# Performance work log

Measured on AMD Instinct MI355X. Metric: run time of the kernel, lower is better.

The kernel has to match this reference:

```python
import jax, jax.numpy as jnp
import numpy as np

HEADS = 8

def _grid_edges(H, W):
    # 4-neighbor grid adjacency, built at trace time (static), faithful to the torch double loop
    N = H * W
    idx = np.arange(N).reshape(H, W)
    e = np.zeros((N, N), np.float32)
    a, b = idx[1:, :].ravel(), idx[:-1, :].ravel()
    e[a, b] = 1.0; e[b, a] = 1.0
    a, b = idx[:, 1:].ravel(), idx[:, :-1].ravel()
    e[a, b] = 1.0; e[b, a] = 1.0
    return jnp.asarray(e)

def _layernorm(x, g, b, eps=1e-5):
    m = x.mean(-1, keepdims=True)
    v = x.var(-1, keepdims=True)
    return (x - m) / jnp.sqrt(v + eps) * g + b

def _gat(nodes, edges, W, b, rel):
    # nodes: [N,B,E]; W: [4,E,E] (q,k,v,out); rel: [HEADS]
    N, B, E = nodes.shape
    hd = E // HEADS
    q = (nodes @ W[0].T + b[0]).reshape(N, B, HEADS, hd)
    k = (nodes @ W[1].T + b[1]).reshape(N, B, HEADS, hd)
    v = (nodes @ W[2].T + b[2]).reshape(N, B, HEADS, hd)
    s = jnp.einsum('ibhd,jbhd->hbij', q, k) / float(np.sqrt(hd))
    s = s + edges[None, None] * rel[:, None, None, None]  # per-head edge relation bias
    a = jax.nn.softmax(s, axis=1)  # faithful to source: softmax over dim=1 (batch axis)
    o = jnp.einsum('hbij,jbhd->ibhd', a, v).reshape(N, B, E)
    return o @ W[3].T + b[3]

def _mha(q_in, kv_in, W, b):
    # standard nn.MultiheadAttention (eval, no dropout); seq-first [L,B,E]
    L, B, E = q_in.shape
    S = kv_in.shape[0]
    hd = E // HEADS
    q = (q_in @ W[0].T + b[0]).reshape(L, B, HEADS, hd)
    k = (kv_in @ W[1].T + b[1]).reshape(S, B, HEADS, hd)
    v = (kv_in @ W[2].T + b[2]).reshape(S, B, HEADS, hd)
    s = jnp.einsum('ibhd,jbhd->hbij', q, k) / float(np.sqrt(hd))
    a = jax.nn.softmax(s, axis=-1)
    o = jnp.einsum('hbij,jbhd->ibhd', a, v).reshape(L, B, E)
    return o @ W[3].T + b[3]

def reference(x, gat_W, gat_b, gat_rel, cross_W, cross_b, ln_g, ln_b):
    B, C, H, W = x.shape
    P = H // 4
    # global nodes: avg_pool2d(kernel=4) then flatten to [P*P, B, C]
    g = x.reshape(B, C, P, 4, P, 4).mean(axis=(3, 5))
    global_nodes = g.reshape(B, C, P * P).transpose(2, 0, 1)
    global_edges = jnp.ones((P * P, P * P), x.dtype)
    local_nodes = x.reshape(B, C, H * W).transpose(2, 0, 1)  # [HW,B,C]
    local_edges = _grid_edges(H, W)
    g_out = _gat(global_nodes, global_edges, gat_W[0], gat_b[0], gat_rel[0])
    g_out = _layernorm(g_out + global_nodes, ln_g[0], ln_b[0])
    l_out = _gat(local_nodes, local_edges, gat_W[1], gat_b[1], gat_rel[1])
    l_out = _layernorm(l_out + local_nodes, ln_g[1], ln_b[1])
    # nearest upsample x4 of global output back to HxW
    g_map = g_out.transpose(1, 2, 0).reshape(B, C, P, P)
    g_up = jnp.repeat(jnp.repeat(g_map, 4, axis=2), 4, axis=3)
    g_up = g_up.reshape(B, C, H * W).transpose(2, 0, 1)
    c_out = _mha(l_out, g_up, cross_W, cross_b)
    c_out = _layernorm(c_out + l_out, ln_g[2], ln_b[2])
    return c_out.transpose(1, 2, 0).reshape(B, C, H, W)

def setup_inputs() -> dict:
    key = jax.random.key(0)
    ks = jax.random.split(key, 6)
    B, C, H, W = 2, 256, 40, 40
    E = C
    sc = 0.02
    return {
        "x": jax.random.normal(ks[0], (B, C, H, W), jnp.float32),
        "gat_W": jax.random.normal(ks[1], (2, 4, E, E), jnp.float32) * sc,
        "gat_b": jax.random.normal(ks[2], (2, 4, E), jnp.float32) * sc,
        "gat_rel": jax.random.normal(ks[3], (2, HEADS), jnp.float32),
        "cross_W": jax.random.normal(ks[4], (4, E, E), jnp.float32) * sc,
        "cross_b": jax.random.normal(ks[5], (4, E), jnp.float32) * sc,
        "ln_g": jnp.ones((3, E), jnp.float32),
        "ln_b": jnp.zeros((3, E), jnp.float32),
    }
```

## Files before the change

kernel.cpp:

```cpp
#include <hip/hip_runtime.h>
#include <math.h>

#define NLOC 1600
#define NGLO 100

typedef unsigned short u16;
typedef short s16x8 __attribute__((ext_vector_type(8)));
typedef float f32x4 __attribute__((ext_vector_type(4)));

__device__ __forceinline__ short f2bf(float f) {
    unsigned u = __float_as_uint(f);
    u += 0x7fffu + ((u >> 16) & 1u);
    return (short)(u >> 16);
}
__device__ __forceinline__ float bf2f(u16 h) {
    return __uint_as_float(((unsigned)h) << 16);
}


__device__ __forceinline__ void gemm_tile(int lane, const u16* __restrict__ A,
                                          const u16* __restrict__ W,
                                          const float* __restrict__ bias,
                                          u16* __restrict__ C, int M, int m0, int n0) {
    int c = lane & 15, qd = lane >> 4;
    f32x4 acc[2][4] = {};
#pragma unroll 2
    for (int kc = 0; kc < 8; ++kc) {
        int ko = kc * 32 + qd * 8;
        s16x8 af[2], bf[4];
#pragma unroll
        for (int mi = 0; mi < 2; ++mi) {
            int row = m0 + mi * 16 + c;
            s16x8 zz = {};
            af[mi] = (row < M) ? *(const s16x8*)(A + (size_t)row * 256 + ko) : zz;
        }
#pragma unroll
        for (int ni = 0; ni < 4; ++ni)
            bf[ni] = *(const s16x8*)(W + (size_t)(n0 + ni * 16 + c) * 256 + ko);
#pragma unroll
        for (int mi = 0; mi < 2; ++mi)
#pragma unroll
            for (int ni = 0; ni < 4; ++ni)
                acc[mi][ni] = __builtin_amdgcn_mfma_f32_16x16x32_bf16(af[mi], bf[ni],
                                                                      acc[mi][ni], 0, 0, 0);
    }
#pragma unroll
    for (int mi = 0; mi < 2; ++mi)
#pragma unroll
        for (int r = 0; r < 4; ++r) {
            int row = m0 + mi * 16 + 4 * qd + r;
            if (row < M) {
#pragma unroll
                for (int ni = 0; ni < 4; ++ni) {
                    int col = n0 + ni * 16 + c;
                    C[(size_t)row * 256 + col] = (u16)f2bf(acc[mi][ni][r] + bias[col]);
                }
            }
        }
}

template <int MODE>
__device__ __forceinline__ void gemmln_block(int tid, const u16* __restrict__ A,
                                             const u16* __restrict__ W,
                                             const float* __restrict__ bias,
                                             const float* __restrict__ R,
                                             const float* __restrict__ g,
                                             const float* __restrict__ bb,
                                             float* fout, u16* bfout, float* dout,
                                             int M, int m0) {
    int w = tid >> 6, lane = tid & 63;
    int c = lane & 15, qd = lane >> 4;
    int n0 = w * 64;

    f32x4 acc[4] = {};
#pragma unroll 2
    for (int kc = 0; kc < 8; ++kc) {
        int ko = kc * 32 + qd * 8;
        int row = m0 + c;
        s16x8 zz = {};
        s16x8 af = (row < M) ? *(const s16x8*)(A + (size_t)row * 256 + ko) : zz;
#pragma unroll
        for (int ni = 0; ni < 4; ++ni) {
            s16x8 bf = *(const s16x8*)(W + (size_t)(n0 + ni * 16 + c) * 256 + ko);
            acc[ni] = __builtin_amdgcn_mfma_f32_16x16x32_bf16(af, bf, acc[ni], 0, 0, 0);
        }
    }

    __shared__ float ps1[4][16], ps2[4][16];
    float v[4][4];
#pragma unroll
    for (int r = 0; r < 4; ++r) {
        int row = m0 + 4 * qd + r;
        bool ok = (row < M);
        float s1 = 0.f, s2 = 0.f;
#pragma unroll
        for (int ni = 0; ni < 4; ++ni) {
            int col = n0 + ni * 16 + c;
            float val = acc[ni][r] + bias[col] + (ok ? R[(size_t)row * 256 + col] : 0.f);
            v[r][ni] = val;
            s1 += val; s2 += val * val;
        }
        s1 += __shfl_xor(s1, 1); s2 += __shfl_xor(s2, 1);
        s1 += __shfl_xor(s1, 2); s2 += __shfl_xor(s2, 2);
        s1 += __shfl_xor(s1, 4); s2 += __shfl_xor(s2, 4);
        s1 += __shfl_xor(s1, 8); s2 += __shfl_xor(s2, 8);
        if (c == 0) { ps1[w][4 * qd + r] = s1; ps2[w][4 * qd + r] = s2; }
    }
    __syncthreads();

    if (MODE == 0) {
#pragma unroll
        for (int r = 0; r < 4; ++r) {
            int lr = 4 * qd + r;
            int row = m0 + lr;
            if (row >= M) continue;
            float s1 = ps1[0][lr] + ps1[1][lr] + ps1[2][lr] + ps1[3][lr];
            float s2 = ps2[0][lr] + ps2[1][lr] + ps2[2][lr] + ps2[3][lr];
            float mean = s1 * (1.f / 256.f);
            float var  = s2 * (1.f / 256.f) - mean * mean;
            float rstd = rsqrtf(var + 1e-5f);
#pragma unroll
            for (int ni = 0; ni < 4; ++ni) {
                int col = n0 + ni * 16 + c;
                float y = (v[r][ni] - mean) * rstd * g[col] + bb[col];
                fout[(size_t)row * 256 + col] = y;
                bfout[(size_t)row * 256 + col] = (u16)f2bf(y);
            }
        }
    } else {
        __shared__ float ytile[2][8][256];
#pragma unroll
        for (int r = 0; r < 4; ++r) {
            int lr = 4 * qd + r;
            float s1 = ps1[0][lr] + ps1[1][lr] + ps1[2][lr] + ps1[3][lr];
            float s2 = ps2[0][lr] + ps2[1][lr] + ps2[2][lr] + ps2[3][lr];
            float mean = s1 * (1.f / 256.f);
            float var  = s2 * (1.f / 256.f) - mean * mean;
            float rstd = rsqrtf(var + 1e-5f);
#pragma unroll
            for (int ni = 0; ni < 4; ++ni) {
                int col = n0 + ni * 16 + c;
                ytile[lr & 1][lr >> 1][col] = (v[r][ni] - mean) * rstd * g[col] + bb[col];
            }
        }
        __syncthreads();
#pragma unroll
        for (int p = tid; p < 512; p += 256) {
            int b = p >> 8, col = p & 255;
            float4 y0, y1;
            y0.x = ytile[b][0][col]; y0.y = ytile[b][1][col];
            y0.z = ytile[b][2][col]; y0.w = ytile[b][3][col];
            y1.x = ytile[b][4][col]; y1.y = ytile[b][5][col];
            y1.z = ytile[b][6][col]; y1.w = ytile[b][7][col];
            size_t o = ((size_t)(b * 256 + col)) * 1600 + (m0 >> 1);
            *(float4*)(dout + o)     = y0;
            *(float4*)(dout + o + 4) = y1;
        }
    }
}

__global__ __launch_bounds__(256) void k_prep(const float* __restrict__ gw,
                                              const float* __restrict__ cw,
                                              u16* __restrict__ gwb,
                                              u16* __restrict__ cwb,
                                              const float* __restrict__ x,
                                              float* __restrict__ nodes,
                                              u16* __restrict__ nodesb,
                                              float* __restrict__ gn,
                                              u16* __restrict__ gnb) {
    int bx = blockIdx.x;
    if (bx < 768) {
        int t = bx * 256 + threadIdx.x;
        const float* src; u16* dst; int idx;
        if (t < 131072) { src = gw; dst = gwb; idx = t; }
        else            { src = cw; dst = cwb; idx = t - 131072; }
        float4 v = ((const float4*)src)[idx];
        ushort4 o;
        o.x = (u16)f2bf(v.x); o.y = (u16)f2bf(v.y);
        o.z = (u16)f2bf(v.z); o.w = (u16)f2bf(v.w);
        ((ushort4*)dst)[idx] = o;
        return;
    }
    int bid = bx - 768;
    if (bid < 3200) {
        int t = bid * 256 + threadIdx.x;
        int c = t & 255;
        int b = (t >> 8) & 1;
        int n = t >> 9;
        float v = x[((size_t)(b * 256 + c)) * 1600 + n];
        nodes[t] = v;
        nodesb[t] = (u16)f2bf(v);
    } else {
        int t = (bid - 3200) * 256 + threadIdx.x;
        int c = t & 255;
        int b = (t >> 8) & 1;
        int n = t >> 9;
        int p = n / 10, qq = n - p * 10;
        const float* xp = x + ((size_t)(b * 256 + c)) * 1600 + (p * 4) * 40 + qq * 4;
        float s = 0.f;
#pragma unroll
        for (int dy = 0; dy < 4; ++dy)
#pragma unroll
            for (int dx = 0; dx < 4; ++dx)
                s += xp[dy * 40 + dx];
        s *= (1.f / 16.f);
        gn[t] = s;
        gnb[t] = (u16)f2bf(s);
    }
}

__global__ __launch_bounds__(64) void k_qkv(const u16* __restrict__ nodesb,
                                            const u16* __restrict__ gnb,
                                            const u16* __restrict__ W1b,
                                            const u16* __restrict__ W0b,
                                            const float* __restrict__ b1,
                                            const float* __restrict__ b0,
                                            u16* __restrict__ qbuf,
                                            u16* __restrict__ gqb,
                                            float* __restrict__ sv1) {
    int lane = threadIdx.x;
    int bx = blockIdx.x, z = blockIdx.z;
    int n0 = blockIdx.y * 64;
    if (bx == 100 && blockIdx.y == 0 && z == 0) {
#pragma unroll
        for (int i = 0; i < 8; ++i) sv1[lane * 8 + i] = 0.f;
    }
    if (bx < 100)
        gemm_tile(lane, nodesb, W1b + (size_t)z * 65536, b1 + z * 256,
                  qbuf + (size_t)z * 819200, 3200, bx * 32, n0);
    else
        gemm_tile(lane, gnb, W0b + (size_t)z * 65536, b0 + z * 256,
                  gqb + (size_t)z * 51200, 200, (bx - 100) * 32, n0);
}

__device__ __forceinline__ void vtrans_block(const u16* __restrict__ src,
                                             u16* __restrict__ dst,
                                             int M, int Npad, int bxx, int byy,
                                             float* sum) {
    __shared__ u16 tile[32][33];
    int m0 = bxx * 32;
    int e0 = byy * 32;
    int tx = threadIdx.x & 31, ty = threadIdx.x >> 5;
#pragma unroll
    for (int k2 = 0; k2 < 4; ++k2) {
        int m = m0 + ty + k2 * 8;
        tile[ty + k2 * 8][tx] = (m < M) ? src[(size_t)m * 256 + e0 + tx] : (u16)0;
    }
    __syncthreads();
    int b = tx >> 4, nl = tx & 15;
    int n = (m0 >> 1) + nl;
    if (n < Npad) {
#pragma unroll
        for (int k2 = 0; k2 < 4; ++k2) {
            int e = e0 + ty + k2 * 8;
            dst[(size_t)(b * 256 + e) * Npad + n] = tile[2 * nl + b][ty + k2 * 8];
        }
    }
    if (threadIdx.x < 32) {
        float s = 0.f;
#pragma unroll
        for (int r = 0; r < 16; ++r) s += bf2f(tile[2 * r + 1][threadIdx.x]);
        atomicAdd(&sum[e0 + threadIdx.x], s);
    }
}

__global__ __launch_bounds__(256) void k_vtrans(const u16* __restrict__ vbuf,
                                                u16* __restrict__ vtb,
                                                const u16* __restrict__ gvb,
                                                u16* __restrict__ gvt,
                                                float* __restrict__ sv1l,
                                                float* __restrict__ sv1g) {
    int bx = blockIdx.x;
    if (bx < 100) vtrans_block(vbuf, vtb, 3200, 1600, bx, blockIdx.y, sv1l);
    else          vtrans_block(gvb, gvt, 200, 128, bx - 100, blockIdx.y, sv1g);
}

__global__ __launch_bounds__(256) void k_attn(
    const u16* __restrict__ qb, const u16* __restrict__ kb,
    const u16* __restrict__ vt, float* __restrict__ pO, float* __restrict__ pT,
    const u16* __restrict__ gqb, const u16* __restrict__ gkb,
    const u16* __restrict__ gvt, const float* __restrict__ sv1g,
    u16* __restrict__ gattb)
{
    __shared__ u16 ks[2][32][40];
    __shared__ u16 vs[2][32][40];
    __shared__ short At4[4][16][40];

    int tid = threadIdx.x;
    int w = tid >> 6, lane = tid & 63;
    int c = lane & 15, qd = lane >> 4;
    int bx = blockIdx.x;

    if (bx < 800) {
        int q4 = bx & 3;
        int hic = bx >> 2;
        int ic = hic % 25, h = hic / 25;
        int hb = h * 32;
        int i0 = ic * 64 + w * 16;
        int jb0 = q4 * 13, jbe = (jb0 + 13 < 50) ? jb0 + 13 : 50;

        const u16* qp = qb + ((size_t)(i0 + c) * 2) * 256 + hb + qd * 8;
        s16x8 qf0 = *(const s16x8*)qp;
        s16x8 qf1 = *(const s16x8*)(qp + 256);
#pragma unroll
        for (int z = 0; z < 8; ++z) qf0[z] ^= (short)0x8000;

        f32x4 o0[2] = {}, t1[2] = {};

        int srow = tid >> 2, part = tid & 3;
        int sjl = srow >> 1, sb = srow & 1;
        int vb_ = srow >> 5, vd = srow & 31;

        for (int jb = jb0; jb < jbe; ++jb) {
            int j0 = jb * 32;
            __syncthreads();
            {
                s16x8 kv = *(const s16x8*)(kb + (size_t)(j0 + sjl) * 512 + sb * 256 + hb + part * 8);
                *(s16x8*)&ks[sb][sjl][part * 8] = kv;
                s16x8 vv = *(const s16x8*)(vt + (size_t)(vb_ * 256 + hb + vd) * 1600 + j0 + part * 8);
                *(s16x8*)&vs[vb_][vd][part * 8] = vv;
            }
            __syncthreads();

            s16x8 kf00 = *(const s16x8*)&ks[0][c][qd * 8];
            s16x8 kf10 = *(const s16x8*)&ks[1][c][qd * 8];
            s16x8 kf01 = *(const s16x8*)&ks[0][16 + c][qd * 8];
            s16x8 kf11 = *(const s16x8*)&ks[1][16 + c][qd * 8];

            f32x4 z4 = {};
            f32x4 sd0 = __builtin_amdgcn_mfma_f32_16x16x32_bf16(qf0, kf00, z4, 0, 0, 0);
            sd0       = __builtin_amdgcn_mfma_f32_16x16x32_bf16(qf1, kf10, sd0, 0, 0, 0);
            f32x4 sd1 = __builtin_amdgcn_mfma_f32_16x16x32_bf16(qf0, kf01, z4, 0, 0, 0);
            sd1       = __builtin_amdgcn_mfma_f32_16x16x32_bf16(qf1, kf11, sd1, 0, 0, 0);
#pragma unroll
            for (int r = 0; r < 4; ++r) {
                float e0v = __expf(sd0[r] * 0.17677669529663687f);
                At4[w][4 * qd + r][c]      = f2bf(__builtin_amdgcn_rcpf(1.f + e0v));
                float e1v = __expf(sd1[r] * 0.17677669529663687f);
                At4[w][4 * qd + r][16 + c] = f2bf(__builtin_amdgcn_rcpf(1.f + e1v));
            }
            asm volatile("s_waitcnt lgkmcnt(0)" ::: "memory");
            s16x8 af = *(const s16x8*)&At4[w][c][qd * 8];

            s16x8 vf00 = *(const s16x8*)&vs[0][c][qd * 8];
            s16x8 vf01 = *(const s16x8*)&vs[0][16 + c][qd * 8];
            s16x8 vf10 = *(const s16x8*)&vs[1][c][qd * 8];
            s16x8 vf11 = *(const s16x8*)&vs[1][16 + c][qd * 8];

            o0[0] = __builtin_amdgcn_mfma_f32_16x16x32_bf16(af, vf00, o0[0], 0, 0, 0);
            o0[1] = __builtin_amdgcn_mfma_f32_16x16x32_bf16(af, vf01, o0[1], 0, 0, 0);
            t1[0] = __builtin_amdgcn_mfma_f32_16x16x32_bf16(af, vf10, t1[0], 0, 0, 0);
            t1[1] = __builtin_amdgcn_mfma_f32_16x16x32_bf16(af, vf11, t1[1], 0, 0, 0);
        }

        size_t base = (size_t)q4 * 409600;
#pragma unroll
        for (int dh = 0; dh < 2; ++dh)
#pragma unroll
            for (int r = 0; r < 4; ++r) {
                size_t idx = base + (size_t)(i0 + 4 * qd + r) * 256 + hb + dh * 16 + c;
                pO[idx] = o0[dh][r];
                pT[idx] = t1[dh][r];
            }
    } else {
        int idx = (bx - 800) * 4 + w;
        int h = idx / 7, it = idx % 7;
        int i0 = it * 16;
        int hb = h * 32;

        s16x8 qf0 = {}, qf1 = {};
        int i = i0 + c;
        if (i < NGLO) {
            const u16* qp = gqb + ((size_t)i * 2) * 256 + hb + qd * 8;
            qf0 = *(const s16x8*)qp;
            qf1 = *(const s16x8*)(qp + 256);
        }
#pragma unroll
        for (int z = 0; z < 8; ++z) qf0[z] ^= (short)0x8000;

        f32x4 o0[2] = {}, t1[2] = {};

        for (int j0 = 0; j0 < NGLO; j0 += 32) {
            s16x8 kf[2][2], vf[2][2];
#pragma unroll
            for (int b = 0; b < 2; ++b)
#pragma unroll
                for (int js = 0; js < 2; ++js) {
                    int j = j0 + js * 16 + c;
                    s16x8 kv = {};
                    if (j < NGLO) kv = *(const s16x8*)(gkb + ((size_t)j * 2 + b) * 256 + hb + qd * 8);
                    kf[b][js] = kv;
                }
#pragma unroll
            for (int b = 0; b < 2; ++b)
#pragma unroll
                for (int dh = 0; dh < 2; ++dh)
                    vf[b][dh] = *(const s16x8*)(gvt + (size_t)(b * 256 + hb + dh * 16 + c) * 128
                                                + j0 + qd * 8);

            f32x4 z4 = {};
            f32x4 sd0 = __builtin_amdgcn_mfma_f32_16x16x32_bf16(qf0, kf[0][0], z4, 0, 0, 0);
            sd0       = __builtin_amdgcn_mfma_f32_16x16x32_bf16(qf1, kf[1][0], sd0, 0, 0, 0);
            f32x4 sd1 = __builtin_amdgcn_mfma_f32_16x16x32_bf16(qf0, kf[0][1], z4, 0, 0, 0);
            sd1       = __builtin_amdgcn_mfma_f32_16x16x32_bf16(qf1, kf[1][1], sd1, 0, 0, 0);
#pragma unroll
            for (int r = 0; r < 4; ++r) {
                float e0v = __expf(sd0[r] * 0.17677669529663687f);
                At4[w][4 * qd + r][c]      = f2bf(__builtin_amdgcn_rcpf(1.f + e0v));
                float e1v = __expf(sd1[r] * 0.17677669529663687f);
                At4[w][4 * qd + r][16 + c] = f2bf(__builtin_amdgcn_rcpf(1.f + e1v));
            }
            asm volatile("s_waitcnt lgkmcnt(0)" ::: "memory");
            s16x8 af = *(const s16x8*)&At4[w][c][qd * 8];
            o0[0] = __builtin_amdgcn_mfma_f32_16x16x32_bf16(af, vf[0][0], o0[0], 0, 0, 0);
            o0[1] = __builtin_amdgcn_mfma_f32_16x16x32_bf16(af, vf[0][1], o0[1], 0, 0, 0);
            t1[0] = __builtin_amdgcn_mfma_f32_16x16x32_bf16(af, vf[1][0], t1[0], 0, 0, 0);
            t1[1] = __builtin_amdgcn_mfma_f32_16x16x32_bf16(af, vf[1][1], t1[1], 0, 0, 0);
        }

#pragma unroll
        for (int dh = 0; dh < 2; ++dh) {
            float sv = sv1g[hb + dh * 16 + c];
#pragma unroll
            for (int r = 0; r < 4; ++r) {
                int ii = i0 + 4 * qd + r;
                if (ii < NGLO) {
                    size_t o = ((size_t)ii * 2) * 256 + hb + dh * 16 + c;
                    gattb[o]       = (u16)f2bf(o0[dh][r]);
                    gattb[o + 256] = (u16)f2bf(sv - t1[dh][r]);
                }
            }
        }
    }
}

__global__ __launch_bounds__(256) void k_combine_gproj(
    const float* __restrict__ pO, const float* __restrict__ pT,
    const float* __restrict__ sv1l, u16* __restrict__ attb,
    const u16* __restrict__ gattb, const u16* __restrict__ W0p,
    const float* __restrict__ b0p, const float* __restrict__ gn,
    const float* __restrict__ ln_g, const float* __restrict__ ln_b,
    float* __restrict__ gout, u16* __restrict__ goutb)
{
    int bx = blockIdx.x;
    if (bx < 400) {
        int t4 = (bx * 256 + threadIdx.x) * 4;
        int e = t4 & 255;
        int i = t4 >> 8;
        float4 o  = *(const float4*)(pO + t4);
        float4 tt = *(const float4*)(pT + t4);
#pragma unroll
        for (int q = 1; q < 4; ++q) {
            float4 a = *(const float4*)(pO + t4 + q * 409600);
            float4 b = *(const float4*)(pT + t4 + q * 409600);
            o.x += a.x; o.y += a.y; o.z += a.z; o.w += a.w;
            tt.x += b.x; tt.y += b.y; tt.z += b.z; tt.w += b.w;
        }
        float4 sv = *(const float4*)(sv1l + e);
        ushort4 w0, w1;
        w0.x = (u16)f2bf(o.x); w0.y = (u16)f2bf(o.y);
        w0.z = (u16)f2bf(o.z); w0.w = (u16)f2bf(o.w);
        w1.x = (u16)f2bf(sv.x - tt.x); w1.y = (u16)f2bf(sv.y - tt.y);
        w1.z = (u16)f2bf(sv.z - tt.z); w1.w = (u16)f2bf(sv.w - tt.w);
        *(ushort4*)(attb + (size_t)i * 512 + e)       = w0;
        *(ushort4*)(attb + (size_t)i * 512 + 256 + e) = w1;
    } else {
        gemmln_block<0>(threadIdx.x, gattb, W0p, b0p, gn, ln_g, ln_b,
                        gout, goutb, (float*)0, 200, (bx - 400) * 16);
    }
}

__global__ __launch_bounds__(256) void k_lproj_ckcv(
    const u16* __restrict__ attb, const u16* __restrict__ W1p,
    const float* __restrict__ b1p, const float* __restrict__ nodes,
    const float* __restrict__ ln_g1, const float* __restrict__ ln_b1,
    float* __restrict__ lout, u16* __restrict__ loutb,
    const u16* __restrict__ goutb, const u16* __restrict__ wckv,
    const float* __restrict__ bckv, u16* __restrict__ ckb)
{
    int bx = blockIdx.x;
    if (bx < 200) {
        gemmln_block<0>(threadIdx.x, attb, W1p, b1p, nodes, ln_g1, ln_b1,
                        lout, loutb, (float*)0, 3200, bx * 16);
    } else {
        int w = threadIdx.x >> 6, lane = threadIdx.x & 63;
        int idx = (bx - 200) * 4 + w;
        int z = idx / 28, rem = idx % 28;
        int m0 = (rem >> 2) * 32, n0 = (rem & 3) * 64;
        gemm_tile(lane, goutb, wckv + (size_t)z * 65536, bckv + z * 256,
                  ckb + (size_t)z * 51200, 200, m0, n0);
    }
}

__global__ __launch_bounds__(256) void k_cq_vtrans(
    const u16* __restrict__ loutb, const u16* __restrict__ wcq,
    const float* __restrict__ bcq, u16* __restrict__ cqb,
    const u16* __restrict__ cvb, u16* __restrict__ cvt)
{
    int bx = blockIdx.x;
    if (bx < 100) {
        int w = threadIdx.x >> 6, lane = threadIdx.x & 63;
        int idx = bx * 4 + w;
        int m0 = (idx % 100) * 32, n0 = (idx / 100) * 64;
        gemm_tile(lane, loutb, wcq, bcq, cqb, 3200, m0, n0);
    } else {
        int bb = bx - 100;
        __shared__ u16 tile[32][33];
        int m0 = (bb & 7) * 32;
        int e0 = (bb >> 3) * 32;
        int tx = threadIdx.x & 31, ty = threadIdx.x >> 5;
#pragma unroll
        for (int k2 = 0; k2 < 4; ++k2) {
            int m = m0 + ty + k2 * 8;
            tile[ty + k2 * 8][tx] = (m < 200) ? cvb[(size_t)m * 256 + e0 + tx] : (u16)0;
        }
        __syncthreads();
        int b = tx >> 4, nl = tx & 15;
        int n = (m0 >> 1) + nl;
#pragma unroll
        for (int k2 = 0; k2 < 4; ++k2) {
            int e = e0 + ty + k2 * 8;
            cvt[(size_t)(b * 256 + e) * 128 + n] = tile[2 * nl + b][ty + k2 * 8];
        }
    }
}

__global__ __launch_bounds__(256) void k_cross(
    const u16* __restrict__ qb, const u16* __restrict__ kb,
    const u16* __restrict__ vt, u16* __restrict__ out)
{
    __shared__ short At[4][16][136];
    int w = threadIdx.x >> 6, lane = threadIdx.x & 63;
    int c  = lane & 15;
    int qd = lane >> 4;
    int idx = blockIdx.x * 4 + w;
    int it = idx % 100;
    int hb2 = idx / 100;
    int h = hb2 >> 1, b = hb2 & 1;
    int i0 = it * 16;
    int hb = h * 32;

    for (int z = lane; z < 16 * 24; z += 64)
        At[w][z / 24][112 + (z % 24)] = 0;

    const u16* qp = qb + ((size_t)(i0 + c) * 2 + b) * 256 + hb + qd * 8;
    s16x8 qf = *(const s16x8*)qp;

    f32x4 s[7];
#pragma unroll
    for (int jt = 0; jt < 7; ++jt) {
        int j = jt * 16 + c;
        s16x8 kf = {};
        if (j < NGLO) kf = *(const s16x8*)(kb + ((size_t)j * 2 + b) * 256 + hb + qd * 8);
        f32x4 z4 = {};
        s[jt] = __builtin_amdgcn_mfma_f32_16x16x32_bf16(qf, kf, z4, 0, 0, 0);
    }
    if (c >= 4) {
#pragma unroll
        for (int r = 0; r < 4; ++r) s[6][r] = -1e30f;
    }
#pragma unroll
    for (int jt = 0; jt < 7; ++jt)
#pragma unroll
        for (int r = 0; r < 4; ++r) s[jt][r] *= 0.17677669529663687f;

    float l[4];
#pragma unroll
    for (int r = 0; r < 4; ++r) {
        float mm = s[0][r];
#pragma unroll
        for (int jt = 1; jt < 7; ++jt) mm = fmaxf(mm, s[jt][r]);
        mm = fmaxf(mm, __shfl_xor(mm, 1));
        mm = fmaxf(mm, __shfl_xor(mm, 2));
        mm = fmaxf(mm, __shfl_xor(mm, 4));
        mm = fmaxf(mm, __shfl_xor(mm, 8));
        float ll = 0.f;
#pragma unroll
        for (int jt = 0; jt < 7; ++jt) {
            float p = __expf(s[jt][r] - mm);
            s[jt][r] = p;
            ll += p;
        }
        ll += __shfl_xor(ll, 1);
        ll += __shfl_xor(ll, 2);
        ll += __shfl_xor(ll, 4);
        ll += __shfl_xor(ll, 8);
        l[r] = ll;
    }
#pragma unroll
    for (int jt = 0; jt < 7; ++jt)
#pragma unroll
        for (int r = 0; r < 4; ++r)
            At[w][4 * qd + r][jt * 16 + c] = f2bf(s[jt][r]);
    asm volatile("s_waitcnt lgkmcnt(0)" ::: "memory");

    f32x4 o[2] = {};
#pragma unroll
    for (int kc = 0; kc < 4; ++kc) {
        s16x8 af = *(const s16x8*)&At[w][c][kc * 32 + qd * 8];
#pragma unroll
        for (int dh = 0; dh < 2; ++dh) {
            s16x8 vf = *(const s16x8*)(vt + (size_t)(b * 256 + hb + dh * 16 + c) * 128
                                       + kc * 32 + qd * 8);
            o[dh] = __builtin_amdgcn_mfma_f32_16x16x32_bf16(af, vf, o[dh], 0, 0, 0);
        }
    }
#pragma unroll
    for (int dh = 0; dh < 2; ++dh)
#pragma unroll
        for (int r = 0; r < 4; ++r) {
            int ii = i0 + 4 * qd + r;
            out[((size_t)ii * 2 + b) * 256 + hb + dh * 16 + c] = (u16)f2bf(o[dh][r] / l[r]);
        }
}

__global__ __launch_bounds__(256) void k_cproj(
    const u16* __restrict__ cattb, const u16* __restrict__ wcp,
    const float* __restrict__ bcp, const float* __restrict__ lout,
    const float* __restrict__ ln_g2, const float* __restrict__ ln_b2,
    float* __restrict__ dout)
{
    gemmln_block<1>(threadIdx.x, cattb, wcp, bcp, lout, ln_g2, ln_b2,
                    (float*)0, (u16*)0, dout, 3200, blockIdx.x * 16);
}

extern "C" void kernel_launch(void* const* d_in, const int* in_sizes, int n_in,
                              void* d_out, int out_size, void* d_ws, size_t ws_size,
                              hipStream_t stream) {
    const float* x        = (const float*)d_in[0];
    const float* gat_W    = (const float*)d_in[1];
    const float* gat_b    = (const float*)d_in[2];
    const float* cross_W  = (const float*)d_in[4];
    const float* cross_b  = (const float*)d_in[5];
    const float* ln_g     = (const float*)d_in[6];
    const float* ln_b     = (const float*)d_in[7];
    float* out = (float*)d_out;

    float* ws    = (float*)d_ws;
    float* nodes = ws;
    float* lout  = nodes + 819200;
    float* proj  = lout  + 819200;
    float* gn    = proj  + 819200;
    float* gprj  = gn    + 51200;
    float* gout  = gprj  + 51200;
    float* sv1l  = gout  + 51200;
    float* sv1g  = sv1l  + 256;
    float* pT    = sv1g  + 256;
    float* pO    = lout;
    u16* wgatb  = (u16*)(pT + 1638400);
    u16* wcrsb  = wgatb + 524288;
    u16* nodesb = wcrsb + 262144;
    u16* qbuf   = nodesb + 819200;
    u16* kbuf   = qbuf + 819200;
    u16* vbuf   = kbuf + 819200;
    u16* vtb    = vbuf + 819200;
    u16* attb   = vtb + 819200;
    u16* gnb    = attb + 819200;
    u16* gqb    = gnb + 51200;
    u16* gkb    = gqb + 51200;
    u16* gvb    = gkb + 51200;
    u16* gvt    = gvb + 51200;
    u16* gattb  = gvt + 65536;
    u16* goutb  = gattb + 51200;
    u16* ckb    = goutb + 51200;
    u16* cvb    = ckb + 51200;
    u16* cvt    = cvb + 51200;
    u16* loutb  = vbuf;
    u16* cqb    = attb;
    u16* cattb  = kbuf;

    const u16* W0b = wgatb;
    const u16* W1b = wgatb + 4 * 65536;
    const float* b0 = gat_b;
    const float* b1 = gat_b + 4 * 256;

    k_prep<<<4168, 256, 0, stream>>>(gat_W, cross_W, wgatb, wcrsb,
                                     x, nodes, nodesb, gn, gnb);
    k_qkv<<<dim3(107, 4, 3), 64, 0, stream>>>(nodesb, gnb, W1b, W0b, b1, b0,
                                              qbuf, gqb, sv1l);
    k_vtrans<<<dim3(108, 8), 256, 0, stream>>>(vbuf, vtb, gvb, gvt, sv1l, sv1g);
    k_attn<<<814, 256, 0, stream>>>(qbuf, kbuf, vtb, pO, pT,
                                    gqb, gkb, gvt, sv1g, gattb);
    k_combine_gproj<<<413, 256, 0, stream>>>(pO, pT, sv1l, attb,
                                             gattb, W0b + 3 * 65536, b0 + 768, gn,
                                             ln_g, ln_b, gout, goutb);
    k_lproj_ckcv<<<214, 256, 0, stream>>>(attb, W1b + 3 * 65536, b1 + 768, nodes,
                                          ln_g + 256, ln_b + 256, lout, loutb,
                                          goutb, wcrsb + 65536, cross_b + 256, ckb);
    k_cq_vtrans<<<164, 256, 0, stream>>>(loutb, wcrsb, cross_b, cqb, cvb, cvt);
    k_cross<<<400, 256, 0, stream>>>(cqb, ckb, cvt, cattb);
    k_cproj<<<200, 256, 0, stream>>>(cattb, wcrsb + 3 * 65536, cross_b + 768, lout,
                                     ln_g + 512, ln_b + 512, out);
}
```

Baseline: 167.0 us.

## Fuse V transposes into GEMM epilogues and cross-Q projection into cross attention

The V-projection GEMMs now write their output already transposed, and the batch-1 column sums are accumulated inside the epilogue. This removes the separate k_vtrans kernel and the transpose half of k_cq_vtrans. The cross-attention Q projection is computed per block inside k_cross, which removes another launch and the cqb round trip. k_prep now uses an LDS-tiled transpose for the node layout, one block per pooled node, and also zeroes the padding and accumulators. The costs are scattered strided 2-byte stores in the transposed epilogue, more atomics, and the Q GEMM being recomputed in every k_cross block that shares the same rows.

Measured after the change: 185.2 us. +10.9%, slower.

```diff
diff --git a/kernel.cpp b/kernel.cpp
--- a/kernel.cpp
+++ b/kernel.cpp
@@ -17,13 +17,14 @@
     return __uint_as_float(((unsigned)h) << 16);
 }
 
-
-__device__ __forceinline__ void gemm_tile(int lane, const u16* __restrict__ A,
+__device__ __forceinline__ void gemm_core(int lane, const u16* __restrict__ A,
                                           const u16* __restrict__ W,
-                                          const float* __restrict__ bias,
-                                          u16* __restrict__ C, int M, int m0, int n0) {
+                                          int M, int m0, int n0, f32x4 acc[2][4]) {
     int c = lane & 15, qd = lane >> 4;
-    f32x4 acc[2][4] = {};
+#pragma unroll
+    for (int mi = 0; mi < 2; ++mi)
+#pragma unroll
+        for (int ni = 0; ni < 4; ++ni) acc[mi][ni] = (f32x4){0.f, 0.f, 0.f, 0.f};
 #pragma unroll 2
     for (int kc = 0; kc < 8; ++kc) {
         int ko = kc * 32 + qd * 8;
@@ -44,6 +45,12 @@
                 acc[mi][ni] = __builtin_amdgcn_mfma_f32_16x16x32_bf16(af[mi], bf[ni],
                                                                       acc[mi][ni], 0, 0, 0);
     }
+}
+
+__device__ __forceinline__ void ep_row(int lane, f32x4 acc[2][4],
+                                       const float* __restrict__ bias,
+                                       u16* __restrict__ C, int M, int m0, int n0) {
+    int c = lane & 15, qd = lane >> 4;
 #pragma unroll
     for (int mi = 0; mi < 2; ++mi)
 #pragma unroll
@@ -57,6 +64,35 @@
                 }
             }
         }
+}
+
+__device__ __forceinline__ void ep_vt(int lane, f32x4 acc[2][4],
+                                      const float* __restrict__ bias,
+                                      u16* __restrict__ vt, int Npad,
+                                      int M, int m0, int n0, float* sum) {
+    int c = lane & 15, qd = lane >> 4;
+    float s[4] = {0.f, 0.f, 0.f, 0.f};
+#pragma unroll
+    for (int mi = 0; mi < 2; ++mi)
+#pragma unroll
+        for (int r = 0; r < 4; ++r) {
+            int row = m0 + mi * 16 + 4 * qd + r;
+            if (row < M) {
+                int n = row >> 1, b = row & 1;
+#pragma unroll
+                for (int ni = 0; ni < 4; ++ni) {
+                    int col = n0 + ni * 16 + c;
+                    float val = acc[mi][ni][r] + bias[col];
+                    vt[(size_t)(b * 256 + col) * Npad + n] = (u16)f2bf(val);
+                    if (b) s[ni] += val;
+                }
+            }
+        }
+    if (sum) {
+#pragma unroll
+        for (int ni = 0; ni < 4; ++ni)
+            atomicAdd(&sum[n0 + ni * 16 + c], s[ni]);
+    }
 }
 
 template <int MODE>
@@ -145,8 +181,8 @@
         }
         __syncthreads();
 #pragma unroll
-        for (int p = tid; p < 512; p += 256) {
-            int b = p >> 8, col = p & 255;
+        for (int pp = tid; pp < 512; pp += 256) {
+            int b = pp >> 8, col = pp & 255;
             float4 y0, y1;
             y0.x = ytile[b][0][col]; y0.y = ytile[b][1][col];
             y0.z = ytile[b][2][col]; y0.w = ytile[b][3][col];
@@ -167,10 +203,14 @@
                                               float* __restrict__ nodes,
                                               u16* __restrict__ nodesb,
                                               float* __restrict__ gn,
-                                              u16* __restrict__ gnb) {
+                                              u16* __restrict__ gnb,
+                                              float* __restrict__ sv1,
+                                              u16* __restrict__ gvt,
+                                              u16* __restrict__ cvt) {
     int bx = blockIdx.x;
+    int tid = threadIdx.x;
     if (bx < 768) {
-        int t = bx * 256 + threadIdx.x;
+        int t = bx * 256 + tid;
         const float* src; u16* dst; int idx;
         if (t < 131072) { src = gw; dst = gwb; idx = t; }
         else            { src = cw; dst = cwb; idx = t - 131072; }
@@ -179,24 +219,33 @@
         o.x = (u16)f2bf(v.x); o.y = (u16)f2bf(v.y);
         o.z = (u16)f2bf(v.z); o.w = (u16)f2bf(v.w);
         ((ushort4*)dst)[idx] = o;
-        return;
-    }
-    int bid = bx - 768;
-    if (bid < 3200) {
-        int t = bid * 256 + threadIdx.x;
-        int c = t & 255;
-        int b = (t >> 8) & 1;
-        int n = t >> 9;
-        float v = x[((size_t)(b * 256 + c)) * 1600 + n];
-        nodes[t] = v;
-        nodesb[t] = (u16)f2bf(v);
-    } else {
-        int t = (bid - 3200) * 256 + threadIdx.x;
-        int c = t & 255;
-        int b = (t >> 8) & 1;
-        int n = t >> 9;
-        int p = n / 10, qq = n - p * 10;
-        const float* xp = x + ((size_t)(b * 256 + c)) * 1600 + (p * 4) * 40 + qq * 4;
+    } else if (bx < 1568) {
+        __shared__ float tile[32][33];
+        int tt = bx - 768;
+        int cb = tt / 100, rem = tt - cb * 100;
+        int nb = rem >> 1, b = rem & 1;
+        int c0 = cb * 32, n0t = nb * 32;
+        int tx = tid & 31, ty = tid >> 5;
+#pragma unroll
+        for (int k2 = 0; k2 < 4; ++k2) {
+            int cc = c0 + ty + k2 * 8;
+            tile[ty + k2 * 8][tx] = x[((size_t)(b * 256 + cc)) * 1600 + n0t + tx];
+        }
+        __syncthreads();
+#pragma unroll
+        for (int k2 = 0; k2 < 4; ++k2) {
+            int n = n0t + ty + k2 * 8;
+            float val = tile[tx][ty + k2 * 8];
+            size_t o = ((size_t)(n * 2 + b)) * 256 + c0 + tx;
+            nodes[o] = val;
+            nodesb[o] = (u16)f2bf(val);
+        }
+    } else if (bx < 1768) {
+        int pt = bx - 1568;
+        int b = pt & 1, n = pt >> 1;
+        int cc = tid;
+        int pr = n / 10, qqc = n - pr * 10;
+        const float* xp = x + ((size_t)(b * 256 + cc)) * 1600 + (pr * 4) * 40 + qqc * 4;
         float s = 0.f;
 #pragma unroll
         for (int dy = 0; dy < 4; ++dy)
@@ -204,8 +253,18 @@
             for (int dx = 0; dx < 4; ++dx)
                 s += xp[dy * 40 + dx];
         s *= (1.f / 16.f);
+        size_t t = (size_t)pt * 256 + cc;
         gn[t] = s;
         gnb[t] = (u16)f2bf(s);
+    } else if (bx == 1768) {
+        sv1[tid] = 0.f;
+        sv1[tid + 256] = 0.f;
+    } else if (bx == 1769) {
+        for (int e2 = tid; e2 < 512; e2 += 256)
+            for (int n = 100; n < 128; ++n) gvt[(size_t)e2 * 128 + n] = 0;
+    } else {
+        for (int e2 = tid; e2 < 512; e2 += 256)
+            for (int n = 100; n < 128; ++n) cvt[(size_t)e2 * 128 + n] = 0;
     }
 }
 
@@ -216,63 +275,32 @@
                                             const float* __restrict__ b1,
                                             const float* __restrict__ b0,
                                             u16* __restrict__ qbuf,
+                                            u16* __restrict__ kbuf,
+                                            u16* __restrict__ vtb,
                                             u16* __restrict__ gqb,
-                                            float* __restrict__ sv1) {
+                                            u16* __restrict__ gkb,
+                                            u16* __restrict__ gvt,
+                                            float* __restrict__ sv1l,
+                                            float* __restrict__ sv1g) {
     int lane = threadIdx.x;
     int bx = blockIdx.x, z = blockIdx.z;
     int n0 = blockIdx.y * 64;
-    if (bx == 100 && blockIdx.y == 0 && z == 0) {
-#pragma unroll
-        for (int i = 0; i < 8; ++i) sv1[lane * 8 + i] = 0.f;
-    }
-    if (bx < 100)
-        gemm_tile(lane, nodesb, W1b + (size_t)z * 65536, b1 + z * 256,
-                  qbuf + (size_t)z * 819200, 3200, bx * 32, n0);
-    else
-        gemm_tile(lane, gnb, W0b + (size_t)z * 65536, b0 + z * 256,
-                  gqb + (size_t)z * 51200, 200, (bx - 100) * 32, n0);
-}
-
-__device__ __forceinline__ void vtrans_block(const u16* __restrict__ src,
-                                             u16* __restrict__ dst,
-                                             int M, int Npad, int bxx, int byy,
-                                             float* sum) {
-    __shared__ u16 tile[32][33];
-    int m0 = bxx * 32;
-    int e0 = byy * 32;
-    int tx = threadIdx.x & 31, ty = threadIdx.x >> 5;
-#pragma unroll
-    for (int k2 = 0; k2 < 4; ++k2) {
-        int m = m0 + ty + k2 * 8;
-        tile[ty + k2 * 8][tx] = (m < M) ? src[(size_t)m * 256 + e0 + tx] : (u16)0;
-    }
-    __syncthreads();
-    int b = tx >> 4, nl = tx & 15;
-    int n = (m0 >> 1) + nl;
-    if (n < Npad) {
-#pragma unroll
-        for (int k2 = 0; k2 < 4; ++k2) {
-            int e = e0 + ty + k2 * 8;
-            dst[(size_t)(b * 256 + e) * Npad + n] = tile[2 * nl + b][ty + k2 * 8];
-        }
-    }
-    if (threadIdx.x < 32) {
-        float s = 0.f;
-#pragma unroll
-        for (int r = 0; r < 16; ++r) s += bf2f(tile[2 * r + 1][threadIdx.x]);
-        atomicAdd(&sum[e0 + threadIdx.x], s);
-    }
-}
-
-__global__ __launch_bounds__(256) void k_vtrans(const u16* __restrict__ vbuf,
-                                                u16* __restrict__ vtb,
-                                                const u16* __restrict__ gvb,
-                                                u16* __restrict__ gvt,
-                                                float* __restrict__ sv1l,
-                                                float* __restrict__ sv1g) {
-    int bx = blockIdx.x;
-    if (bx < 100) vtrans_block(vbuf, vtb, 3200, 1600, bx, blockIdx.y, sv1l);
-    else          vtrans_block(gvb, gvt, 200, 128, bx - 100, blockIdx.y, sv1g);
+    f32x4 acc[2][4];
+    if (bx < 100) {
+        int m0 = bx * 32;
+        gemm_core(lane, nodesb, W1b + (size_t)z * 65536, 3200, m0, n0, acc);
+        const float* bias = b1 + z * 256;
+        if (z == 0)      ep_row(lane, acc, bias, qbuf, 3200, m0, n0);
+        else if (z == 1) ep_row(lane, acc, bias, kbuf, 3200, m0, n0);
+        else             ep_vt(lane, acc, bias, vtb, 1600, 3200, m0, n0, sv1l);
+    } else {
+        int m0 = (bx - 100) * 32;
+        gemm_core(lane, gnb, W0b + (size_t)z * 65536, 200, m0, n0, acc);
+        const float* bias = b0 + z * 256;
+        if (z == 0)      ep_row(lane, acc, bias, gqb, 200, m0, n0);
+        else if (z == 1) ep_row(lane, acc, bias, gkb, 200, m0, n0);
+        else             ep_vt(lane, acc, bias, gvt, 128, 200, m0, n0, sv1g);
+    }
 }
 
 __global__ __launch_bounds__(256) void k_attn(
@@ -476,7 +504,8 @@
     const float* __restrict__ ln_g1, const float* __restrict__ ln_b1,
     float* __restrict__ lout, u16* __restrict__ loutb,
     const u16* __restrict__ goutb, const u16* __restrict__ wckv,
-    const float* __restrict__ bckv, u16* __restrict__ ckb)
+    const float* __restrict__ bckv, u16* __restrict__ ckb,
+    u16* __restrict__ cvt)
 {
     int bx = blockIdx.x;
     if (bx < 200) {
@@ -485,51 +514,25 @@
     } else {
         int w = threadIdx.x >> 6, lane = threadIdx.x & 63;
         int idx = (bx - 200) * 4 + w;
-        int z = idx / 28, rem = idx % 28;
-        int m0 = (rem >> 2) * 32, n0 = (rem & 3) * 64;
-        gemm_tile(lane, goutb, wckv + (size_t)z * 65536, bckv + z * 256,
-                  ckb + (size_t)z * 51200, 200, m0, n0);
-    }
-}
-
-__global__ __launch_bounds__(256) void k_cq_vtrans(
+        if (idx < 56) {
+            int z = idx / 28, rem = idx % 28;
+            int m0 = (rem >> 2) * 32, n0 = (rem & 3) * 64;
+            f32x4 acc[2][4];
+            gemm_core(lane, goutb, wckv + (size_t)z * 65536, 200, m0, n0, acc);
+            const float* bias = bckv + z * 256;
+            if (z == 0) ep_row(lane, acc, bias, ckb, 200, m0, n0);
+            else        ep_vt(lane, acc, bias, cvt, 128, 200, m0, n0, (float*)0);
+        }
+    }
+}
+
+__global__ __launch_bounds__(256) void k_cross(
     const u16* __restrict__ loutb, const u16* __restrict__ wcq,
-    const float* __restrict__ bcq, u16* __restrict__ cqb,
-    const u16* __restrict__ cvb, u16* __restrict__ cvt)
-{
-    int bx = blockIdx.x;
-    if (bx < 100) {
-        int w = threadIdx.x >> 6, lane = threadIdx.x & 63;
-        int idx = bx * 4 + w;
-        int m0 = (idx % 100) * 32, n0 = (idx / 100) * 64;
-        gemm_tile(lane, loutb, wcq, bcq, cqb, 3200, m0, n0);
-    } else {
-        int bb = bx - 100;
-        __shared__ u16 tile[32][33];
-        int m0 = (bb & 7) * 32;
-        int e0 = (bb >> 3) * 32;
-        int tx = threadIdx.x & 31, ty = threadIdx.x >> 5;
-#pragma unroll
-        for (int k2 = 0; k2 < 4; ++k2) {
-            int m = m0 + ty + k2 * 8;
-            tile[ty + k2 * 8][tx] = (m < 200) ? cvb[(size_t)m * 256 + e0 + tx] : (u16)0;
-        }
-        __syncthreads();
-        int b = tx >> 4, nl = tx & 15;
-        int n = (m0 >> 1) + nl;
-#pragma unroll
-        for (int k2 = 0; k2 < 4; ++k2) {
-            int e = e0 + ty + k2 * 8;
-            cvt[(size_t)(b * 256 + e) * 128 + n] = tile[2 * nl + b][ty + k2 * 8];
-        }
-    }
-}
-
-__global__ __launch_bounds__(256) void k_cross(
-    const u16* __restrict__ qb, const u16* __restrict__ kb,
+    const float* __restrict__ bcq, const u16* __restrict__ kb,
     const u16* __restrict__ vt, u16* __restrict__ out)
 {
     __shared__ short At[4][16][136];
+    __shared__ short Aq[4][16][40];
     int w = threadIdx.x >> 6, lane = threadIdx.x & 63;
     int c  = lane & 15;
     int qd = lane >> 4;
@@ -543,8 +546,24 @@
     for (int z = lane; z < 16 * 24; z += 64)
         At[w][z / 24][112 + (z % 24)] = 0;
 
-    const u16* qp = qb + ((size_t)(i0 + c) * 2 + b) * 256 + hb + qd * 8;
-    s16x8 qf = *(const s16x8*)qp;
+    f32x4 qacc[2] = {};
+#pragma unroll 2
+    for (int kc = 0; kc < 8; ++kc) {
+        int ko = kc * 32 + qd * 8;
+        s16x8 af = *(const s16x8*)(loutb + ((size_t)(i0 + c) * 2 + b) * 256 + ko);
+#pragma unroll
+        for (int ni = 0; ni < 2; ++ni) {
+            s16x8 bf = *(const s16x8*)(wcq + (size_t)(hb + ni * 16 + c) * 256 + ko);
+            qacc[ni] = __builtin_amdgcn_mfma_f32_16x16x32_bf16(af, bf, qacc[ni], 0, 0, 0);
+        }
+    }
+#pragma unroll
+    for (int ni = 0; ni < 2; ++ni)
+#pragma unroll
+        for (int r = 0; r < 4; ++r)
+            Aq[w][4 * qd + r][ni * 16 + c] = f2bf(qacc[ni][r] + bcq[hb + ni * 16 + c]);
+    asm volatile("s_waitcnt lgkmcnt(0)" ::: "memory");
+    s16x8 qf = *(const s16x8*)&Aq[w][c][qd * 8];
 
     f32x4 s[7];
 #pragma unroll
@@ -577,9 +596,9 @@
         float ll = 0.f;
 #pragma unroll
         for (int jt = 0; jt < 7; ++jt) {
-            float p = __expf(s[jt][r] - mm);
-            s[jt][r] = p;
-            ll += p;
+            float pv = __expf(s[jt][r] - mm);
+            s[jt][r] = pv;
+            ll += pv;
         }
         ll += __shfl_xor(ll, 1);
         ll += __shfl_xor(ll, 2);
@@ -638,35 +657,31 @@
 
     float* ws    = (float*)d_ws;
     float* nodes = ws;
-    float* lout  = nodes + 819200;
-    float* proj  = lout  + 819200;
-    float* gn    = proj  + 819200;
-    float* gprj  = gn    + 51200;
-    float* gout  = gprj  + 51200;
-    float* sv1l  = gout  + 51200;
-    float* sv1g  = sv1l  + 256;
-    float* pT    = sv1g  + 256;
-    float* pO    = lout;
-    u16* wgatb  = (u16*)(pT + 1638400);
-    u16* wcrsb  = wgatb + 524288;
-    u16* nodesb = wcrsb + 262144;
-    u16* qbuf   = nodesb + 819200;
-    u16* kbuf   = qbuf + 819200;
-    u16* vbuf   = kbuf + 819200;
-    u16* vtb    = vbuf + 819200;
-    u16* attb   = vtb + 819200;
-    u16* gnb    = attb + 819200;
-    u16* gqb    = gnb + 51200;
-    u16* gkb    = gqb + 51200;
-    u16* gvb    = gkb + 51200;
-    u16* gvt    = gvb + 51200;
-    u16* gattb  = gvt + 65536;
-    u16* goutb  = gattb + 51200;
-    u16* ckb    = goutb + 51200;
-    u16* cvb    = ckb + 51200;
-    u16* cvt    = cvb + 51200;
-    u16* loutb  = vbuf;
-    u16* cqb    = attb;
+    float* gn    = nodes + 819200;
+    float* gout  = gn + 51200;
+    float* lout  = gout + 51200;
+    float* sv1l  = lout + 819200;
+    float* sv1g  = sv1l + 256;
+    float* pO    = sv1g + 256;
+    float* pT    = pO + 1638400;
+
+    u16* ub = (u16*)(pT + 1638400);
+    u16* wgatb  = ub;            ub += 524288;
+    u16* wcrsb  = ub;            ub += 262144;
+    u16* nodesb = ub;            ub += 819200;
+    u16* gnb    = ub;            ub += 51200;
+    u16* qbuf   = ub;            ub += 819200;
+    u16* kbuf   = ub;            ub += 819200;
+    u16* vtb    = ub;            ub += 819200;
+    u16* gqb    = ub;            ub += 51200;
+    u16* gkb    = ub;            ub += 51200;
+    u16* gvt    = ub;            ub += 65536;
+    u16* gattb  = ub;            ub += 51200;
+    u16* goutb  = ub;            ub += 51200;
+    u16* attb   = ub;            ub += 819200;
+    u16* loutb  = ub;            ub += 819200;
+    u16* ckb    = ub;            ub += 51200;
+    u16* cvt    = ub;            ub += 65536;
     u16* cattb  = kbuf;
 
     const u16* W0b = wgatb;
@@ -674,11 +689,11 @@
     const float* b0 = gat_b;
     const float* b1 = gat_b + 4 * 256;
 
-    k_prep<<<4168, 256, 0, stream>>>(gat_W, cross_W, wgatb, wcrsb,
-                                     x, nodes, nodesb, gn, gnb);
+    k_prep<<<1771, 256, 0, stream>>>(gat_W, cross_W, wgatb, wcrsb,
+                                     x, nodes, nodesb, gn, gnb, sv1l, gvt, cvt);
     k_qkv<<<dim3(107, 4, 3), 64, 0, stream>>>(nodesb, gnb, W1b, W0b, b1, b0,
-                                              qbuf, gqb, sv1l);
-    k_vtrans<<<dim3(108, 8), 256, 0, stream>>>(vbuf, vtb, gvb, gvt, sv1l, sv1g);
+                                              qbuf, kbuf, vtb, gqb, gkb, gvt,
+                                              sv1l, sv1g);
     k_attn<<<814, 256, 0, stream>>>(qbuf, kbuf, vtb, pO, pT,
                                     gqb, gkb, gvt, sv1g, gattb);
     k_combine_gproj<<<413, 256, 0, stream>>>(pO, pT, sv1l, attb,
@@ -686,9 +701,9 @@
                                              ln_g, ln_b, gout, goutb);
     k_lproj_ckcv<<<214, 256, 0, stream>>>(attb, W1b + 3 * 65536, b1 + 768, nodes,
                                           ln_g + 256, ln_b + 256, lout, loutb,
-                                          goutb, wcrsb + 65536, cross_b + 256, ckb);
-    k_cq_vtrans<<<164, 256, 0, stream>>>(loutb, wcrsb, cross_b, cqb, cvb, cvt);
-    k_cross<<<400, 256, 0, stream>>>(cqb, ckb, cvt, cattb);
+                                          goutb, wcrsb + 65536, cross_b + 256,
+                                          ckb, cvt);
+    k_cross<<<400, 256, 0, stream>>>(loutb, wcrsb, cross_b, ckb, cvt, cattb);
     k_cproj<<<200, 256, 0, stream>>>(cattb, wcrsb + 3 * 65536, cross_b + 768, lout,
                                      ln_g + 512, ln_b + 512, out);
 }
```
